# Kernel tuning notes

Measured on AMD Instinct MI355X. Metric: run time of the kernel, lower is better.

## Reference

```python
import jax, jax.numpy as jnp
import numpy as np

B, S, T = 32, 32, 64          # docs, sentences/doc, tokens/sentence
E, HW, HS = 128, 128, 128     # embed, word hidden, sentence hidden
CW, CS = 128, 128             # attention context sizes
V, NC = 50000, 8              # vocab, classes


def setup_inputs() -> dict:
    key = jax.random.key(0)
    ks = iter(jax.random.split(key, 40))
    x = jax.random.randint(next(ks), (B, S, T), 1, V, dtype=jnp.int32)
    wl = jax.random.randint(next(ks), (B, S), 8, T + 1)   # word lengths
    sl = jax.random.randint(next(ks), (B,), 8, S + 1)     # sentence counts
    tmask = jnp.arange(T)[None, None, :] < wl[:, :, None]
    smask = (jnp.arange(S)[None, :] < sl[:, None])[:, :, None]
    x = jnp.where(tmask & smask, x, 0)                     # 0 = pad token

    def u(shape, scale=0.1):
        return jax.random.uniform(next(ks), shape, jnp.float32, -scale, scale)

    d = {"x": x, "emb": u((V, E))}
    # GRU params in torch layout: W_ih [3H,D] (r|z|n), W_hh [3H,H], biases [3H]
    for pre, Din, H in [("wf", E, HW), ("wb", E, HW), ("sf", 2 * HW, HS), ("sb", 2 * HW, HS)]:
        d[pre + "_Wih"] = u((3 * H, Din))
        d[pre + "_Whh"] = u((3 * H, H))
        d[pre + "_bih"] = u((3 * H,))
        d[pre + "_bhh"] = u((3 * H,))
    d["wproj_W"] = u((CW, 2 * HW)); d["wproj_b"] = u((CW,)); d["wctx"] = u((CW,))
    d["sproj_W"] = u((CS, 2 * HS)); d["sproj_b"] = u((CS,)); d["sctx"] = u((CS,))
    d["fc_W"] = u((NC, 2 * HS)); d["fc_b"] = u((NC,))
    return d


def seq_lens_2d(tok):
    # torch get_sequence_lens: T - trailing zeros, 1 if all zero
    nz = tok != 0
    any_nz = jnp.any(nz, axis=1)
    last = tok.shape[1] - jnp.argmax(nz[:, ::-1], axis=1)
    return jnp.where(any_nz, last, 1)


def doc_lens(x):
    # torch get_num_sentences_lens: S - trailing all-zero sentences
    nz = jnp.any(x != 0, axis=2)  # [B,S]
    any_nz = jnp.any(nz, axis=1)
    last = x.shape[1] - jnp.argmax(nz[:, ::-1], axis=1)
    return jnp.where(any_nz, last, 1)


def run_gru(x, lens, Wih, Whh, bih, bhh, reverse):
    # x: [N,Tm,D]; emulates pack_padded: state frozen / output zeroed beyond len
    N, Tm, _ = x.shape
    H = Whh.shape[1]
    xp = jnp.einsum('ntd,gd->ntg', x, Wih) + bih  # [N,Tm,3H]

    def step(h, inp):
        xg, t = inp
        hg = h @ Whh.T + bhh
        xr, xz, xn = jnp.split(xg, 3, axis=-1)
        hr, hz, hn = jnp.split(hg, 3, axis=-1)
        r = jax.nn.sigmoid(xr + hr)
        z = jax.nn.sigmoid(xz + hz)
        n = jnp.tanh(xn + r * hn)
        h_new = (1 - z) * n + z * h
        valid = (t < lens)[:, None]
        h_new = jnp.where(valid, h_new, h)
        return h_new, jnp.where(valid, h_new, 0.0)

    h0 = jnp.zeros((N, H), x.dtype)
    _, ys = jax.lax.scan(step, h0, (jnp.swapaxes(xp, 0, 1), jnp.arange(Tm)), reverse=reverse)
    return jnp.swapaxes(ys, 0, 1)  # [N,Tm,H]


def bigru(x, lens, pf, pb):
    return jnp.concatenate([run_gru(x, lens, *pf, reverse=False),
                            run_gru(x, lens, *pb, reverse=True)], axis=-1)


def attn_pool(out, lens, Wp, bp, ctx):
    # faithful to torch: softmax over padded positions up to max(lens)
    # (pad_packed pads to max length; padded outputs are zero but score=tanh(b)@c)
    Tm = out.shape[1]
    scores = jnp.tanh(out @ Wp.T + bp) @ ctx            # [N,Tm]
    valid = jnp.arange(Tm)[None, :] < jnp.max(lens)
    attn = jax.nn.softmax(jnp.where(valid, scores, -jnp.inf), axis=-1)
    return jnp.einsum('nt,nth->nh', attn, out)


def han_forward(x, emb,
                wf_Wih, wf_Whh, wf_bih, wf_bhh, wb_Wih, wb_Whh, wb_bih, wb_bhh,
                wproj_W, wproj_b, wctx,
                sf_Wih, sf_Whh, sf_bih, sf_bhh, sb_Wih, sb_Whh, sb_bih, sb_bhh,
                sproj_W, sproj_b, sctx, fc_W, fc_b):
    Bx, Sx, Tx = x.shape
    xw = x.reshape(-1, Tx)                      # [B*S, T]
    wlens = seq_lens_2d(xw)
    slens = doc_lens(x)
    we = emb[xw]                                # [B*S, T, E]
    wout = bigru(we, wlens, (wf_Wih, wf_Whh, wf_bih, wf_bhh),
                 (wb_Wih, wb_Whh, wb_bih, wb_bhh))     # [B*S, T, 2HW]
    sent = attn_pool(wout, wlens, wproj_W, wproj_b, wctx)  # [B*S, 2HW]
    sent = sent.reshape(Bx, Sx, -1)
    sout = bigru(sent, slens, (sf_Wih, sf_Whh, sf_bih, sf_bhh),
                 (sb_Wih, sb_Whh, sb_bih, sb_bhh))     # [B, S, 2HS]
    doc = attn_pool(sout, slens, sproj_W, sproj_b, sctx)   # [B, 2HS]
    return doc @ fc_W.T + fc_b                             # [B, NC]


def reference(x, emb,
              wf_Wih, wf_Whh, wf_bih, wf_bhh, wb_Wih, wb_Whh, wb_bih, wb_bhh,
              wproj_W, wproj_b, wctx,
              sf_Wih, sf_Whh, sf_bih, sf_bhh, sb_Wih, sb_Whh, sb_bih, sb_bhh,
              sproj_W, sproj_b, sctx, fc_W, fc_b):
    return han_forward(x, emb,
                       wf_Wih, wf_Whh, wf_bih, wf_bhh, wb_Wih, wb_Whh, wb_bih, wb_bhh,
                       wproj_W, wproj_b, wctx,
                       sf_Wih, sf_Whh, sf_bih, sf_bhh, sb_Wih, sb_Whh, sb_bih, sb_bhh,
                       sproj_W, sproj_b, sctx, fc_W, fc_b)
```

## Files before the change

### kernel.cpp

```cpp
#include <hip/hip_runtime.h>
#include <hip/hip_bf16.h>

typedef unsigned short ushort_t;
typedef __attribute__((ext_vector_type(4))) float floatx4;
typedef __attribute__((ext_vector_type(8))) short short8;

__device__ __forceinline__ float bf2f(ushort_t u) {
    union { unsigned int i; float f; } v; v.i = ((unsigned int)u) << 16; return v.f;
}
__device__ __forceinline__ ushort_t f2bf(float f) {
    union { float f; unsigned int i; } v; v.f = f;
    unsigned int i = v.i;
    i += 0x7fffu + ((i >> 16) & 1u);
    return (ushort_t)(i >> 16);
}
__device__ __forceinline__ float fsig(float x)  { return 1.f / (1.f + __expf(-x)); }
__device__ __forceinline__ float ftanh(float x) { return 1.f - 2.f / (__expf(2.f * x) + 1.f); }

__device__ __forceinline__ floatx4 MFMA16(short8 a, short8 b, floatx4 c) {
    return __builtin_amdgcn_mfma_f32_16x16x32_bf16(a, b, c, 0, 0, 0);
}

__device__ __forceinline__ void bar_lds() {
    asm volatile("s_waitcnt lgkmcnt(0)" ::: "memory");
    __builtin_amdgcn_s_barrier();
}

#define XIDX(c, m) ((((c) * 16) + ((m) ^ ((c) & 15))) * 8)

__global__ __launch_bounds__(64) void lens_kernel(const int* __restrict__ x,
                                                  const unsigned int* __restrict__ raw,
                                                  int* wlens, int* slens, int* dmax,
                                                  int* flag) {
    int b = blockIdx.x, s = threadIdx.x;
    if (b == 32) {
        int c = 0;
        for (int i = 0; i < 16; ++i) {
            unsigned int v = raw[s * 16 + i];
            unsigned int e = (v >> 7) & 0xFFu;
            if (e > 0x7Bu) ++c;
        }
        c += __shfl_xor(c, 1);  c += __shfl_xor(c, 2);  c += __shfl_xor(c, 4);
        c += __shfl_xor(c, 8);  c += __shfl_xor(c, 16); c += __shfl_xor(c, 32);
        if (s == 0) *flag = (c > 64) ? 1 : 0;
        return;
    }
    int last = 0;
    if (s < 32) {
        const int* tok = x + (b * 32 + s) * 64;
        for (int t = 0; t < 64; t += 4) {
            int4 v = *(const int4*)(tok + t);
            if (v.x) last = t + 1;
            if (v.y) last = t + 2;
            if (v.z) last = t + 3;
            if (v.w) last = t + 4;
        }
        wlens[b * 32 + s] = last ? last : 1;
    }
    int len = (s < 32) ? (last ? last : 1) : 0;
    int lm = len;
    for (int off = 32; off; off >>= 1) lm = max(lm, __shfl_xor(lm, off));
    unsigned long long mask = __ballot(s < 32 && last > 0);
    if (s == 0) {
        slens[b] = mask ? (63 - (int)__clzll(mask) + 1) : 1;
        dmax[b] = lm;
    }
}

struct ConvArgs {
    const void* src[25];
    int dstoff[25];
    int count[25];
    int cumblk[26];
};

__global__ __launch_bounds__(256) void convert_kernel(ConvArgs a, ushort_t* __restrict__ dst,
                                                      const int* __restrict__ flag) {
    int b = blockIdx.x;
    int lo = 0, hi = 24;
    while (lo < hi) { int mid = (lo + hi + 1) >> 1; if (a.cumblk[mid] <= b) lo = mid; else hi = mid - 1; }
    int j = lo;
    size_t base = (size_t)(b - a.cumblk[j]) * 2048 + (size_t)threadIdx.x * 8;
    if (base >= (size_t)a.count[j]) return;
    ushort_t* out = dst + a.dstoff[j] + base;
    if (*flag) {
        const float* s = (const float*)a.src[j] + base;
        float4 v0 = *(const float4*)s;
        float4 v1 = *(const float4*)(s + 4);
        union { ushort_t u[8]; uint4 v; } o;
        o.u[0] = f2bf(v0.x); o.u[1] = f2bf(v0.y); o.u[2] = f2bf(v0.z); o.u[3] = f2bf(v0.w);
        o.u[4] = f2bf(v1.x); o.u[5] = f2bf(v1.y); o.u[6] = f2bf(v1.z); o.u[7] = f2bf(v1.w);
        *(uint4*)out = o.v;
    } else {
        *(uint4*)out = *(const uint4*)((const ushort_t*)a.src[j] + base);
    }
}

__global__ __launch_bounds__(512, 2) void word_gru_kernel(
        const int* __restrict__ x, const ushort_t* __restrict__ emb,
        const ushort_t* __restrict__ Wih_f, const ushort_t* __restrict__ Whh_f,
        const ushort_t* __restrict__ bih_f, const ushort_t* __restrict__ bhh_f,
        const ushort_t* __restrict__ Wih_b, const ushort_t* __restrict__ Whh_b,
        const ushort_t* __restrict__ bih_b, const ushort_t* __restrict__ bhh_b,
        const int* __restrict__ lens, ushort_t* __restrict__ out) {
    const int T = 64;
    __shared__ ushort_t h_buf[2][2048];
    __shared__ ushort_t x_buf[2][2048];
    __shared__ float bsum_lds[256];
    __shared__ float bihn_lds[128];
    __shared__ float bhhn_lds[128];
    __shared__ int tok_lds[1024];

    int tid = threadIdx.x;
    int d = blockIdx.y;
    int n0 = blockIdx.x * 16;
    const ushort_t* Wih = d ? Wih_b : Wih_f;
    const ushort_t* Whh = d ? Whh_b : Whh_f;
    const ushort_t* bih = d ? bih_b : bih_f;
    const ushort_t* bhh = d ? bhh_b : bhh_f;
    int lane = tid & 63, wave = tid >> 6;
    int l15 = lane & 15, l4 = (lane >> 4) & 3;
    int jt = wave * 16;
    int j0 = jt + l4 * 4;

    ((int2*)tok_lds)[tid] = ((const int2*)(x + n0 * 64))[tid];
    if (tid < 256) bsum_lds[tid] = bf2f(bih[tid]) + bf2f(bhh[tid]);
    else if (tid < 384) {
        bihn_lds[tid - 256] = bf2f(bih[tid]);
        bhhn_lds[tid - 256] = bf2f(bhh[tid]);
    }
    { uint2 z = {0u, 0u}; *(uint2*)&h_buf[0][tid * 4] = z; }

    short8 wr[4], wz[4], wn[4], ur[4], uz[4], un[4];
    #pragma unroll
    for (int kf = 0; kf < 4; ++kf) {
        int col = kf * 32 + l4 * 8;
        wr[kf] = *(const short8*)(Wih + (size_t)(jt + l15) * 128 + col);
        wz[kf] = *(const short8*)(Wih + (size_t)(128 + jt + l15) * 128 + col);
        wn[kf] = *(const short8*)(Wih + (size_t)(256 + jt + l15) * 128 + col);
        ur[kf] = *(const short8*)(Whh + (size_t)(jt + l15) * 128 + col);
        uz[kf] = *(const short8*)(Whh + (size_t)(128 + jt + l15) * 128 + col);
        un[kf] = *(const short8*)(Whh + (size_t)(256 + jt + l15) * 128 + col);
    }
    __syncthreads();

    floatx4 br  = *(floatx4*)&bsum_lds[j0];
    floatx4 bz  = *(floatx4*)&bsum_lds[128 + j0];
    floatx4 bxn = *(floatx4*)&bihn_lds[j0];
    floatx4 bhn = *(floatx4*)&bhhn_lds[j0];
    int lv = lens[n0 + l15];
    float hreg[4] = {0.f, 0.f, 0.f, 0.f};

    int m_s = tid >> 4, c_s = tid & 15;
    if (tid < 256) {
        int t0 = d ? (T - 1) : 0;
        int tok = tok_lds[m_s * 64 + t0];
        uint4 v = *(const uint4*)(emb + (size_t)tok * 128 + c_s * 8);
        *(uint4*)&x_buf[0][XIDX(c_s, m_s)] = v;
    }
    __syncthreads();

    for (int ti = 0; ti < T; ++ti) {
        int t = d ? (T - 1 - ti) : ti;
        int cur = ti & 1;
        uint4 xnext;
        bool have_next = (ti + 1) < T;
        if (tid < 256 && have_next) {
            int tn = d ? (T - 2 - ti) : (ti + 1);
            xnext = *(const uint4*)(emb + (size_t)tok_lds[m_s * 64 + tn] * 128 + c_s * 8);
        }
        short8 xb[4], hb[4];
        #pragma unroll
        for (int kf = 0; kf < 4; ++kf) {
            xb[kf] = *(const short8*)&x_buf[cur][XIDX(kf * 4 + l4, l15)];
            hb[kf] = *(const short8*)&h_buf[cur][XIDX(kf * 4 + l4, l15)];
        }
        floatx4 arx = br, azx = bz, axn = bxn;
        floatx4 arh = {0.f, 0.f, 0.f, 0.f}, azh = {0.f, 0.f, 0.f, 0.f}, ahn = bhn;
        #pragma unroll
        for (int kf = 0; kf < 4; ++kf) {
            arx = MFMA16(wr[kf], xb[kf], arx);
            azx = MFMA16(wz[kf], xb[kf], azx);
            axn = MFMA16(wn[kf], xb[kf], axn);
        }
        #pragma unroll
        for (int kf = 0; kf < 4; ++kf) {
            arh = MFMA16(ur[kf], hb[kf], arh);
            azh = MFMA16(uz[kf], hb[kf], azh);
            ahn = MFMA16(un[kf], hb[kf], ahn);
        }
        bool valid = t < lv;
        ushort_t hu[4], ou[4];
        #pragma unroll
        for (int i = 0; i < 4; ++i) {
            float r  = fsig(arx[i] + arh[i]);
            float z  = fsig(azx[i] + azh[i]);
            float nn = ftanh(axn[i] + r * ahn[i]);
            float hv = valid ? (nn + z * (hreg[i] - nn)) : hreg[i];
            hreg[i] = hv;
            hu[i] = f2bf(hv);
            ou[i] = valid ? hu[i] : (ushort_t)0;
        }
        ushort4 h4; h4.x = hu[0]; h4.y = hu[1]; h4.z = hu[2]; h4.w = hu[3];
        ushort4 o4; o4.x = ou[0]; o4.y = ou[1]; o4.z = ou[2]; o4.w = ou[3];
        *(ushort4*)&h_buf[cur ^ 1][XIDX(j0 >> 3, l15) + (j0 & 7)] = h4;
        *(ushort4*)(out + ((size_t)(n0 + l15) * T + t) * 256 + d * 128 + j0) = o4;
        if (tid < 256 && have_next)
            *(uint4*)&x_buf[cur ^ 1][XIDX(c_s, m_s)] = xnext;
        bar_lds();
    }
}

__global__ __launch_bounds__(512, 1) void sent_gru_kernel(
        const ushort_t* __restrict__ sent,
        const ushort_t* __restrict__ Wih_f, const ushort_t* __restrict__ Whh_f,
        const ushort_t* __restrict__ bih_f, const ushort_t* __restrict__ bhh_f,
        const ushort_t* __restrict__ Wih_b, const ushort_t* __restrict__ Whh_b,
        const ushort_t* __restrict__ bih_b, const ushort_t* __restrict__ bhh_b,
        const int* __restrict__ lens, ushort_t* __restrict__ out) {
    const int T = 32;
    __shared__ ushort_t h_buf[2][2048];
    __shared__ ushort_t x_buf[2][4096];
    __shared__ float bsum_lds[256];
    __shared__ float bihn_lds[128];
    __shared__ float bhhn_lds[128];

    int tid = threadIdx.x;
    int d = blockIdx.y;
    int n0 = blockIdx.x * 16;
    const ushort_t* Wih = d ? Wih_b : Wih_f;
    const ushort_t* Whh = d ? Whh_b : Whh_f;
    const ushort_t* bih = d ? bih_b : bih_f;
    const ushort_t* bhh = d ? bhh_b : bhh_f;
    int lane = tid & 63, wave = tid >> 6;
    int l15 = lane & 15, l4 = (lane >> 4) & 3;
    int jt = wave * 16;
    int j0 = jt + l4 * 4;

    if (tid < 256) bsum_lds[tid] = bf2f(bih[tid]) + bf2f(bhh[tid]);
    else if (tid < 384) {
        bihn_lds[tid - 256] = bf2f(bih[tid]);
        bhhn_lds[tid - 256] = bf2f(bhh[tid]);
    }
    { uint2 z = {0u, 0u}; *(uint2*)&h_buf[0][tid * 4] = z; }

    short8 wr[8], wz[8], wn[8];
    #pragma unroll
    for (int kf = 0; kf < 8; ++kf) {
        int col = kf * 32 + l4 * 8;
        wr[kf] = *(const short8*)(Wih + (size_t)(jt + l15) * 256 + col);
        wz[kf] = *(const short8*)(Wih + (size_t)(128 + jt + l15) * 256 + col);
        wn[kf] = *(const short8*)(Wih + (size_t)(256 + jt + l15) * 256 + col);
    }
    short8 ur[4], uz[4], un[4];
    #pragma unroll
    for (int kf = 0; kf < 4; ++kf) {
        int col = kf * 32 + l4 * 8;
        ur[kf] = *(const short8*)(Whh + (size_t)(jt + l15) * 128 + col);
        uz[kf] = *(const short8*)(Whh + (size_t)(128 + jt + l15) * 128 + col);
        un[kf] = *(const short8*)(Whh + (size_t)(256 + jt + l15) * 128 + col);
    }
    __syncthreads();

    floatx4 br  = *(floatx4*)&bsum_lds[j0];
    floatx4 bz  = *(floatx4*)&bsum_lds[128 + j0];
    floatx4 bxn = *(floatx4*)&bihn_lds[j0];
    floatx4 bhn = *(floatx4*)&bhhn_lds[j0];
    int lv = lens[n0 + l15];
    float hreg[4] = {0.f, 0.f, 0.f, 0.f};

    int m_x = tid >> 5, c_x = tid & 31;
    {
        int t0 = d ? (T - 1) : 0;
        uint4 v = *(const uint4*)(sent + ((size_t)(n0 + m_x) * T + t0) * 256 + c_x * 8);
        *(uint4*)&x_buf[0][XIDX(c_x, m_x)] = v;
    }
    __syncthreads();

    for (int ti = 0; ti < T; ++ti) {
        int t = d ? (T - 1 - ti) : ti;
        int cur = ti & 1;
        uint4 xnext;
        bool have_next = (ti + 1) < T;
        if (have_next) {
            int tn = d ? (T - 2 - ti) : (ti + 1);
            xnext = *(const uint4*)(sent + ((size_t)(n0 + m_x) * T + tn) * 256 + c_x * 8);
        }
        floatx4 arx = br, azx = bz, axn = bxn;
        floatx4 arh = {0.f, 0.f, 0.f, 0.f}, azh = {0.f, 0.f, 0.f, 0.f}, ahn = bhn;
        #pragma unroll
        for (int kf = 0; kf < 8; ++kf) {
            short8 xb = *(const short8*)&x_buf[cur][XIDX(kf * 4 + l4, l15)];
            arx = MFMA16(wr[kf], xb, arx);
            azx = MFMA16(wz[kf], xb, azx);
            axn = MFMA16(wn[kf], xb, axn);
        }
        #pragma unroll
        for (int kf = 0; kf < 4; ++kf) {
            short8 hb = *(const short8*)&h_buf[cur][XIDX(kf * 4 + l4, l15)];
            arh = MFMA16(ur[kf], hb, arh);
            azh = MFMA16(uz[kf], hb, azh);
            ahn = MFMA16(un[kf], hb, ahn);
        }
        bool valid = t < lv;
        ushort_t hu[4], ou[4];
        #pragma unroll
        for (int i = 0; i < 4; ++i) {
            float r  = fsig(arx[i] + arh[i]);
            float z  = fsig(azx[i] + azh[i]);
            float nn = ftanh(axn[i] + r * ahn[i]);
            float hv = valid ? (nn + z * (hreg[i] - nn)) : hreg[i];
            hreg[i] = hv;
            hu[i] = f2bf(hv);
            ou[i] = valid ? hu[i] : (ushort_t)0;
        }
        ushort4 h4; h4.x = hu[0]; h4.y = hu[1]; h4.z = hu[2]; h4.w = hu[3];
        ushort4 o4; o4.x = ou[0]; o4.y = ou[1]; o4.z = ou[2]; o4.w = ou[3];
        *(ushort4*)&h_buf[cur ^ 1][XIDX(j0 >> 3, l15) + (j0 & 7)] = h4;
        *(ushort4*)(out + ((size_t)(n0 + l15) * T + t) * 256 + d * 128 + j0) = o4;
        if (have_next)
            *(uint4*)&x_buf[cur ^ 1][XIDX(c_x, m_x)] = xnext;
        bar_lds();
    }
}

#define SP 264
__global__ __launch_bounds__(256) void word_attn_kernel(const ushort_t* __restrict__ wout,
                                                        const ushort_t* __restrict__ W,
                                                        const ushort_t* __restrict__ bias,
                                                        const ushort_t* __restrict__ ctx,
                                                        const int* __restrict__ dmax,
                                                        ushort_t* __restrict__ sent) {
    __shared__ ushort_t tile[64 * SP];
    __shared__ float bc[256];
    __shared__ float sc_lds[64];
    __shared__ float p_lds[64];
    int tid = threadIdx.x, g = blockIdx.x;
    for (int idx = tid; idx < 2048; idx += 256) {
        int row = idx >> 5, k0 = (idx & 31) * 8;
        *(uint4*)&tile[row * SP + k0] = *(const uint4*)(wout + ((size_t)g * 64 + row) * 256 + k0);
    }
    if (tid < 128) bc[tid] = bf2f(bias[tid]);
    else bc[tid] = bf2f(ctx[tid - 128]);
    __syncthreads();
    int lane = tid & 63, wave = tid >> 6;
    int l15 = lane & 15, l4 = (lane >> 4) & 3;
    short8 a[8];
    #pragma unroll
    for (int kf = 0; kf < 8; ++kf)
        a[kf] = *(const short8*)&tile[(wave * 16 + l15) * SP + kf * 32 + l4 * 8];
    floatx4 acc[8];
    #pragma unroll
    for (int nt = 0; nt < 8; ++nt) {
        floatx4 c = {0.f, 0.f, 0.f, 0.f};
        #pragma unroll
        for (int kf = 0; kf < 8; ++kf) {
            short8 b = *(const short8*)(W + (size_t)(nt * 16 + l15) * 256 + kf * 32 + l4 * 8);
            c = MFMA16(a[kf], b, c);
        }
        acc[nt] = c;
    }
    float s[4] = {0.f, 0.f, 0.f, 0.f};
    #pragma unroll
    for (int nt = 0; nt < 8; ++nt) {
        float bv = bc[nt * 16 + l15], cv = bc[128 + nt * 16 + l15];
        #pragma unroll
        for (int i = 0; i < 4; ++i)
            s[i] += ftanh(acc[nt][i] + bv) * cv;
    }
    #pragma unroll
    for (int i = 0; i < 4; ++i) {
        s[i] += __shfl_xor(s[i], 1);
        s[i] += __shfl_xor(s[i], 2);
        s[i] += __shfl_xor(s[i], 4);
        s[i] += __shfl_xor(s[i], 8);
    }
    if (l15 == 0) {
        #pragma unroll
        for (int i = 0; i < 4; ++i) sc_lds[wave * 16 + l4 * 4 + i] = s[i];
    }
    __syncthreads();
    if (tid < 64) {
        int ml = dmax[tid & 31];
        for (int off = 32; off; off >>= 1) ml = max(ml, __shfl_xor(ml, off));
        bool v = tid < ml;
        float sc = v ? sc_lds[tid] : -1e30f;
        float mx = sc;
        for (int off = 32; off; off >>= 1) mx = fmaxf(mx, __shfl_xor(mx, off));
        float e = v ? __expf(sc - mx) : 0.f;
        float sum = e;
        for (int off = 32; off; off >>= 1) sum += __shfl_xor(sum, off);
        p_lds[tid] = e / fmaxf(sum, 1e-30f);
    }
    __syncthreads();
    float acc2 = 0.f;
    for (int t = 0; t < 64; ++t) acc2 += p_lds[t] * bf2f(tile[t * SP + tid]);
    sent[(size_t)g * 256 + tid] = f2bf(acc2);
}

__global__ __launch_bounds__(256) void sent_attn_fc_kernel(const ushort_t* __restrict__ sout,
                                                           const ushort_t* __restrict__ W,
                                                           const ushort_t* __restrict__ bias,
                                                           const ushort_t* __restrict__ ctx,
                                                           const ushort_t* __restrict__ fcW,
                                                           const ushort_t* __restrict__ fcb,
                                                           const int* __restrict__ slens,
                                                           const int* __restrict__ flagp,
                                                           void* __restrict__ outp) {
    __shared__ ushort_t tile[32 * SP];
    __shared__ float bc[256];
    __shared__ float sc_lds[32];
    __shared__ float p_lds[32];
    __shared__ float dv[256];
    int tid = threadIdx.x, g = blockIdx.x;
    for (int idx = tid; idx < 1024; idx += 256) {
        int row = idx >> 5, k0 = (idx & 31) * 8;
        *(uint4*)&tile[row * SP + k0] = *(const uint4*)(sout + ((size_t)g * 32 + row) * 256 + k0);
    }
    if (tid < 128) bc[tid] = bf2f(bias[tid]);
    else bc[tid] = bf2f(ctx[tid - 128]);
    __syncthreads();
    int lane = tid & 63, wave = tid >> 6;
    int l15 = lane & 15, l4 = (lane >> 4) & 3;
    if (wave < 2) {
        short8 a[8];
        #pragma unroll
        for (int kf = 0; kf < 8; ++kf)
            a[kf] = *(const short8*)&tile[(wave * 16 + l15) * SP + kf * 32 + l4 * 8];
        floatx4 acc[8];
        #pragma unroll
        for (int nt = 0; nt < 8; ++nt) {
            floatx4 c = {0.f, 0.f, 0.f, 0.f};
            #pragma unroll
            for (int kf = 0; kf < 8; ++kf) {
                short8 b = *(const short8*)(W + (size_t)(nt * 16 + l15) * 256 + kf * 32 + l4 * 8);
                c = MFMA16(a[kf], b, c);
            }
            acc[nt] = c;
        }
        float s[4] = {0.f, 0.f, 0.f, 0.f};
        #pragma unroll
        for (int nt = 0; nt < 8; ++nt) {
            float bv = bc[nt * 16 + l15], cv = bc[128 + nt * 16 + l15];
            #pragma unroll
            for (int i = 0; i < 4; ++i)
                s[i] += ftanh(acc[nt][i] + bv) * cv;
        }
        #pragma unroll
        for (int i = 0; i < 4; ++i) {
            s[i] += __shfl_xor(s[i], 1);
            s[i] += __shfl_xor(s[i], 2);
            s[i] += __shfl_xor(s[i], 4);
            s[i] += __shfl_xor(s[i], 8);
        }
        if (l15 == 0) {
            #pragma unroll
            for (int i = 0; i < 4; ++i) sc_lds[wave * 16 + l4 * 4 + i] = s[i];
        }
    }
    __syncthreads();
    if (tid < 32) {
        int ml = slens[tid];
        for (int off = 16; off; off >>= 1) ml = max(ml, __shfl_xor(ml, off, 32));
        bool v = tid < ml;
        float sc = v ? sc_lds[tid] : -1e30f;
        float mx = sc;
        for (int off = 16; off; off >>= 1) mx = fmaxf(mx, __shfl_xor(mx, off, 32));
        float e = v ? __expf(sc - mx) : 0.f;
        float sum = e;
        for (int off = 16; off; off >>= 1) sum += __shfl_xor(sum, off, 32);
        p_lds[tid] = e / fmaxf(sum, 1e-30f);
    }
    __syncthreads();
    float acc2 = 0.f;
    for (int t = 0; t < 32; ++t) acc2 += p_lds[t] * bf2f(tile[t * SP + tid]);
    dv[tid] = acc2;
    __syncthreads();
    int c = tid >> 5, q0 = (tid & 31) * 8;
    float partial = 0.f;
    #pragma unroll
    for (int q = 0; q < 8; ++q)
        partial += dv[q0 + q] * bf2f(fcW[(size_t)c * 256 + q0 + q]);
    for (int off = 16; off; off >>= 1) partial += __shfl_xor(partial, off, 32);
    if ((tid & 31) == 0) {
        float v = partial + bf2f(fcb[c]);
        if (*flagp) ((float*)outp)[g * 8 + c] = v;
        else        ((ushort_t*)outp)[g * 8 + c] = f2bf(v);
    }
}

extern "C" void kernel_launch(void* const* d_in, const int* in_sizes, int n_in,
                              void* d_out, int out_size, void* d_ws, size_t ws_size,
                              hipStream_t stream) {
    const int* x = (const int*)d_in[0];
    char* ws = (char*)d_ws;

    const size_t O_CONV = 0;
    const size_t O_WOUT = 14680064;
    const size_t O_SENT = 48234496;
    const size_t O_SOUT = 48758784;
    const size_t O_LENS = 49283072;
    const size_t O_SLEN = 49287168;
    const size_t O_DMAX = 49287296;
    const size_t O_FLAG = 49287424;

    ushort_t* conv = (ushort_t*)(ws + O_CONV);
    ushort_t* wout = (ushort_t*)(ws + O_WOUT);
    ushort_t* sent = (ushort_t*)(ws + O_SENT);
    ushort_t* sout = (ushort_t*)(ws + O_SOUT);
    int* wlens = (int*)(ws + O_LENS);
    int* slens = (int*)(ws + O_SLEN);
    int* dmax  = (int*)(ws + O_DMAX);
    int* flag  = (int*)(ws + O_FLAG);

    ConvArgs ca;
    ushort_t* cw[25];
    int off = 0, blk = 0;
    for (int i = 1; i <= 25; ++i) {
        int j = i - 1;
        int cnt = in_sizes[i];
        ca.src[j] = d_in[i];
        ca.dstoff[j] = off;
        ca.count[j] = cnt;
        ca.cumblk[j] = blk;
        cw[j] = conv + off;
        off += cnt;
        blk += (cnt + 2047) / 2048;
    }
    ca.cumblk[25] = blk;

    lens_kernel<<<33, 64, 0, stream>>>(x, (const unsigned int*)d_in[1],
                                       wlens, slens, dmax, flag);
    convert_kernel<<<blk, 256, 0, stream>>>(ca, conv, flag);
    word_gru_kernel<<<dim3(64, 2), 512, 0, stream>>>(
        x, cw[0],
        cw[1], cw[2], cw[3], cw[4],
        cw[5], cw[6], cw[7], cw[8],
        wlens, wout);
    word_attn_kernel<<<1024, 256, 0, stream>>>(wout, cw[17], cw[18], cw[19], dmax, sent);
    sent_gru_kernel<<<dim3(2, 2), 512, 0, stream>>>(
        sent,
        cw[9], cw[10], cw[11], cw[12],
        cw[13], cw[14], cw[15], cw[16],
        slens, sout);
    sent_attn_fc_kernel<<<32, 256, 0, stream>>>(sout, cw[20], cw[21], cw[22],
                                                cw[23], cw[24], slens, flag, d_out);
    (void)n_in; (void)out_size; (void)ws_size;
}
```

Measured before the change: 322.6 us.

## Hoist sentence GRU input projection into parallel GEMM and deepen word-GRU prefetch

```diff
diff --git a/kernel.cpp b/kernel.cpp
--- a/kernel.cpp
+++ b/kernel.cpp
@@ -105,7 +105,7 @@
         const int* __restrict__ lens, ushort_t* __restrict__ out) {
     const int T = 64;
     __shared__ ushort_t h_buf[2][2048];
-    __shared__ ushort_t x_buf[2][2048];
+    __shared__ ushort_t x_buf[3][2048];
     __shared__ float bsum_lds[256];
     __shared__ float bihn_lds[128];
     __shared__ float bhhn_lds[128];
@@ -152,28 +152,31 @@
     float hreg[4] = {0.f, 0.f, 0.f, 0.f};
 
     int m_s = tid >> 4, c_s = tid & 15;
-    if (tid < 256) {
+    bool stg = tid < 256;
+    uint4 pend1, pend2;
+    if (stg) {
         int t0 = d ? (T - 1) : 0;
-        int tok = tok_lds[m_s * 64 + t0];
-        uint4 v = *(const uint4*)(emb + (size_t)tok * 128 + c_s * 8);
+        uint4 v = *(const uint4*)(emb + (size_t)tok_lds[m_s * 64 + t0] * 128 + c_s * 8);
         *(uint4*)&x_buf[0][XIDX(c_s, m_s)] = v;
+    }
+    if (stg && T > 1) {
+        int t1 = d ? (T - 2) : 1;
+        pend1 = *(const uint4*)(emb + (size_t)tok_lds[m_s * 64 + t1] * 128 + c_s * 8);
     }
     __syncthreads();
 
     for (int ti = 0; ti < T; ++ti) {
         int t = d ? (T - 1 - ti) : ti;
-        int cur = ti & 1;
-        uint4 xnext;
-        bool have_next = (ti + 1) < T;
-        if (tid < 256 && have_next) {
-            int tn = d ? (T - 2 - ti) : (ti + 1);
-            xnext = *(const uint4*)(emb + (size_t)tok_lds[m_s * 64 + tn] * 128 + c_s * 8);
+        int cur = ti % 3;
+        if (stg && (ti + 2) < T) {
+            int tn = d ? (T - 3 - ti) : (ti + 2);
+            pend2 = *(const uint4*)(emb + (size_t)tok_lds[m_s * 64 + tn] * 128 + c_s * 8);
         }
         short8 xb[4], hb[4];
         #pragma unroll
         for (int kf = 0; kf < 4; ++kf) {
             xb[kf] = *(const short8*)&x_buf[cur][XIDX(kf * 4 + l4, l15)];
-            hb[kf] = *(const short8*)&h_buf[cur][XIDX(kf * 4 + l4, l15)];
+            hb[kf] = *(const short8*)&h_buf[ti & 1][XIDX(kf * 4 + l4, l15)];
         }
         floatx4 arx = br, azx = bz, axn = bxn;
         floatx4 arh = {0.f, 0.f, 0.f, 0.f}, azh = {0.f, 0.f, 0.f, 0.f}, ahn = bhn;
@@ -203,55 +206,100 @@
         }
         ushort4 h4; h4.x = hu[0]; h4.y = hu[1]; h4.z = hu[2]; h4.w = hu[3];
         ushort4 o4; o4.x = ou[0]; o4.y = ou[1]; o4.z = ou[2]; o4.w = ou[3];
-        *(ushort4*)&h_buf[cur ^ 1][XIDX(j0 >> 3, l15) + (j0 & 7)] = h4;
+        *(ushort4*)&h_buf[(ti & 1) ^ 1][XIDX(j0 >> 3, l15) + (j0 & 7)] = h4;
         *(ushort4*)(out + ((size_t)(n0 + l15) * T + t) * 256 + d * 128 + j0) = o4;
-        if (tid < 256 && have_next)
-            *(uint4*)&x_buf[cur ^ 1][XIDX(c_s, m_s)] = xnext;
+        if (stg && (ti + 1) < T) {
+            *(uint4*)&x_buf[(ti + 1) % 3][XIDX(c_s, m_s)] = pend1;
+            pend1 = pend2;
+        }
         bar_lds();
     }
 }
 
+__global__ __launch_bounds__(256) void spt_gemm_kernel(const ushort_t* __restrict__ A,
+                                                       const ushort_t* __restrict__ Bf_,
+                                                       const ushort_t* __restrict__ biasf,
+                                                       ushort_t* __restrict__ Tf_,
+                                                       const ushort_t* __restrict__ Bb_,
+                                                       const ushort_t* __restrict__ biasb,
+                                                       ushort_t* __restrict__ Tb_) {
+    __shared__ ushort_t As[64 * 256];
+    __shared__ ushort_t Bs[64 * 256];
+    const int K = 256;
+    int tid = threadIdx.x;
+    int by = blockIdx.y;
+    bool sb = by >= 6;
+    int n0 = (sb ? by - 6 : by) * 64;
+    const ushort_t* B = sb ? Bb_ : Bf_;
+    const ushort_t* bias = sb ? biasb : biasf;
+    ushort_t* Tp = sb ? Tb_ : Tf_;
+    int m0 = blockIdx.x * 64;
+    for (int idx = tid; idx < 2048; idx += 256) {
+        int m = idx & 63, c = idx >> 6;
+        *(uint4*)&As[(c * 64 + m) * 8] = *(const uint4*)(A + (size_t)(m0 + m) * K + c * 8);
+    }
+    for (int idx = tid; idx < 2048; idx += 256) {
+        int n = idx & 63, c = idx >> 6;
+        *(uint4*)&Bs[(c * 64 + n) * 8] = *(const uint4*)(B + (size_t)(n0 + n) * K + c * 8);
+    }
+    __syncthreads();
+    int lane = tid & 63, wave = tid >> 6;
+    int wm = (wave & 1) * 32, wn = (wave >> 1) * 32;
+    int l15 = lane & 15, l4 = lane >> 4;
+    floatx4 acc[2][2] = {};
+    for (int kf = 0; kf < 8; ++kf) {
+        int c = kf * 4 + l4;
+        short8 a0 = *(const short8*)&As[(c * 64 + wm + l15) * 8];
+        short8 a1 = *(const short8*)&As[(c * 64 + wm + 16 + l15) * 8];
+        short8 b0 = *(const short8*)&Bs[(c * 64 + wn + l15) * 8];
+        short8 b1 = *(const short8*)&Bs[(c * 64 + wn + 16 + l15) * 8];
+        acc[0][0] = MFMA16(a0, b0, acc[0][0]);
+        acc[0][1] = MFMA16(a0, b1, acc[0][1]);
+        acc[1][0] = MFMA16(a1, b0, acc[1][0]);
+        acc[1][1] = MFMA16(a1, b1, acc[1][1]);
+    }
+    for (int nt = 0; nt < 2; ++nt) {
+        int n = n0 + wn + nt * 16 + l15;
+        float bv = bf2f(bias[n]);
+        int jc = n >> 2, ji = n & 3;
+        for (int mt = 0; mt < 2; ++mt) {
+            int mbase = m0 + wm + mt * 16 + l4 * 4;
+            #pragma unroll
+            for (int i = 0; i < 4; ++i) {
+                int m = mbase + i;
+                int doc = m >> 5, t = m & 31;
+                size_t dst = ((size_t)((doc >> 4) * 32 + t) * 96 + jc) * 64
+                           + (doc & 15) * 4 + ji;
+                Tp[dst] = f2bf(acc[mt][nt][i] + bv);
+            }
+        }
+    }
+}
+
 __global__ __launch_bounds__(512, 1) void sent_gru_kernel(
-        const ushort_t* __restrict__ sent,
-        const ushort_t* __restrict__ Wih_f, const ushort_t* __restrict__ Whh_f,
-        const ushort_t* __restrict__ bih_f, const ushort_t* __restrict__ bhh_f,
-        const ushort_t* __restrict__ Wih_b, const ushort_t* __restrict__ Whh_b,
-        const ushort_t* __restrict__ bih_b, const ushort_t* __restrict__ bhh_b,
+        const ushort_t* __restrict__ spT_f, const ushort_t* __restrict__ spT_b,
+        const ushort_t* __restrict__ Whh_f, const ushort_t* __restrict__ Whh_b,
+        const ushort_t* __restrict__ bhh_f, const ushort_t* __restrict__ bhh_b,
         const int* __restrict__ lens, ushort_t* __restrict__ out) {
     const int T = 32;
     __shared__ ushort_t h_buf[2][2048];
-    __shared__ ushort_t x_buf[2][4096];
-    __shared__ float bsum_lds[256];
-    __shared__ float bihn_lds[128];
-    __shared__ float bhhn_lds[128];
+    __shared__ float bhh_lds[384];
 
     int tid = threadIdx.x;
     int d = blockIdx.y;
     int n0 = blockIdx.x * 16;
-    const ushort_t* Wih = d ? Wih_b : Wih_f;
+    const ushort_t* spT = d ? spT_b : spT_f;
     const ushort_t* Whh = d ? Whh_b : Whh_f;
-    const ushort_t* bih = d ? bih_b : bih_f;
     const ushort_t* bhh = d ? bhh_b : bhh_f;
     int lane = tid & 63, wave = tid >> 6;
     int l15 = lane & 15, l4 = (lane >> 4) & 3;
     int jt = wave * 16;
     int j0 = jt + l4 * 4;
-
-    if (tid < 256) bsum_lds[tid] = bf2f(bih[tid]) + bf2f(bhh[tid]);
-    else if (tid < 384) {
-        bihn_lds[tid - 256] = bf2f(bih[tid]);
-        bhhn_lds[tid - 256] = bf2f(bhh[tid]);
-    }
+    int jc = j0 >> 2;
+
+    if (tid < 384) bhh_lds[tid] = bf2f(bhh[tid]);
     { uint2 z = {0u, 0u}; *(uint2*)&h_buf[0][tid * 4] = z; }
 
-    short8 wr[8], wz[8], wn[8];
-    #pragma unroll
-    for (int kf = 0; kf < 8; ++kf) {
-        int col = kf * 32 + l4 * 8;
-        wr[kf] = *(const short8*)(Wih + (size_t)(jt + l15) * 256 + col);
-        wz[kf] = *(const short8*)(Wih + (size_t)(128 + jt + l15) * 256 + col);
-        wn[kf] = *(const short8*)(Wih + (size_t)(256 + jt + l15) * 256 + col);
-    }
     short8 ur[4], uz[4], un[4];
     #pragma unroll
     for (int kf = 0; kf < 4; ++kf) {
@@ -262,53 +310,51 @@
     }
     __syncthreads();
 
-    floatx4 br  = *(floatx4*)&bsum_lds[j0];
-    floatx4 bz  = *(floatx4*)&bsum_lds[128 + j0];
-    floatx4 bxn = *(floatx4*)&bihn_lds[j0];
-    floatx4 bhn = *(floatx4*)&bhhn_lds[j0];
+    floatx4 br  = *(floatx4*)&bhh_lds[j0];
+    floatx4 bz  = *(floatx4*)&bhh_lds[128 + j0];
+    floatx4 bhn = *(floatx4*)&bhh_lds[256 + j0];
     int lv = lens[n0 + l15];
     float hreg[4] = {0.f, 0.f, 0.f, 0.f};
 
-    int m_x = tid >> 5, c_x = tid & 31;
+    const ushort_t* sp = spT + (size_t)(blockIdx.x * 32) * 96 * 64 + l15 * 4;
+    ushort4 xr_c, xz_c, xn_c, xr_n, xz_n, xn_n;
     {
         int t0 = d ? (T - 1) : 0;
-        uint4 v = *(const uint4*)(sent + ((size_t)(n0 + m_x) * T + t0) * 256 + c_x * 8);
-        *(uint4*)&x_buf[0][XIDX(c_x, m_x)] = v;
-    }
-    __syncthreads();
+        size_t rb = (size_t)t0 * 96 * 64;
+        xr_c = *(const ushort4*)(sp + rb + (size_t)jc * 64);
+        xz_c = *(const ushort4*)(sp + rb + (size_t)(32 + jc) * 64);
+        xn_c = *(const ushort4*)(sp + rb + (size_t)(64 + jc) * 64);
+    }
 
     for (int ti = 0; ti < T; ++ti) {
         int t = d ? (T - 1 - ti) : ti;
         int cur = ti & 1;
-        uint4 xnext;
         bool have_next = (ti + 1) < T;
         if (have_next) {
             int tn = d ? (T - 2 - ti) : (ti + 1);
-            xnext = *(const uint4*)(sent + ((size_t)(n0 + m_x) * T + tn) * 256 + c_x * 8);
-        }
-        floatx4 arx = br, azx = bz, axn = bxn;
-        floatx4 arh = {0.f, 0.f, 0.f, 0.f}, azh = {0.f, 0.f, 0.f, 0.f}, ahn = bhn;
-        #pragma unroll
-        for (int kf = 0; kf < 8; ++kf) {
-            short8 xb = *(const short8*)&x_buf[cur][XIDX(kf * 4 + l4, l15)];
-            arx = MFMA16(wr[kf], xb, arx);
-            azx = MFMA16(wz[kf], xb, azx);
-            axn = MFMA16(wn[kf], xb, axn);
-        }
+            size_t rb = (size_t)tn * 96 * 64;
+            xr_n = *(const ushort4*)(sp + rb + (size_t)jc * 64);
+            xz_n = *(const ushort4*)(sp + rb + (size_t)(32 + jc) * 64);
+            xn_n = *(const ushort4*)(sp + rb + (size_t)(64 + jc) * 64);
+        }
+        floatx4 ar = br, az = bz, ahn = bhn;
         #pragma unroll
         for (int kf = 0; kf < 4; ++kf) {
             short8 hb = *(const short8*)&h_buf[cur][XIDX(kf * 4 + l4, l15)];
-            arh = MFMA16(ur[kf], hb, arh);
-            azh = MFMA16(uz[kf], hb, azh);
+            ar  = MFMA16(ur[kf], hb, ar);
+            az  = MFMA16(uz[kf], hb, az);
             ahn = MFMA16(un[kf], hb, ahn);
         }
+        float xr[4] = {bf2f(xr_c.x), bf2f(xr_c.y), bf2f(xr_c.z), bf2f(xr_c.w)};
+        float xz[4] = {bf2f(xz_c.x), bf2f(xz_c.y), bf2f(xz_c.z), bf2f(xz_c.w)};
+        float xn[4] = {bf2f(xn_c.x), bf2f(xn_c.y), bf2f(xn_c.z), bf2f(xn_c.w)};
         bool valid = t < lv;
         ushort_t hu[4], ou[4];
         #pragma unroll
         for (int i = 0; i < 4; ++i) {
-            float r  = fsig(arx[i] + arh[i]);
-            float z  = fsig(azx[i] + azh[i]);
-            float nn = ftanh(axn[i] + r * ahn[i]);
+            float r  = fsig(xr[i] + ar[i]);
+            float z  = fsig(xz[i] + az[i]);
+            float nn = ftanh(xn[i] + r * ahn[i]);
             float hv = valid ? (nn + z * (hreg[i] - nn)) : hreg[i];
             hreg[i] = hv;
             hu[i] = f2bf(hv);
@@ -318,8 +364,7 @@
         ushort4 o4; o4.x = ou[0]; o4.y = ou[1]; o4.z = ou[2]; o4.w = ou[3];
         *(ushort4*)&h_buf[cur ^ 1][XIDX(j0 >> 3, l15) + (j0 & 7)] = h4;
         *(ushort4*)(out + ((size_t)(n0 + l15) * T + t) * 256 + d * 128 + j0) = o4;
-        if (have_next)
-            *(uint4*)&x_buf[cur ^ 1][XIDX(c_x, m_x)] = xnext;
+        if (have_next) { xr_c = xr_n; xz_c = xz_n; xn_c = xn_n; }
         bar_lds();
     }
 }
@@ -499,15 +544,19 @@
     const size_t O_WOUT = 14680064;
     const size_t O_SENT = 48234496;
     const size_t O_SOUT = 48758784;
-    const size_t O_LENS = 49283072;
-    const size_t O_SLEN = 49287168;
-    const size_t O_DMAX = 49287296;
-    const size_t O_FLAG = 49287424;
+    const size_t O_SPTF = 49283072;
+    const size_t O_SPTB = 50855936;
+    const size_t O_LENS = 52428800;
+    const size_t O_SLEN = 52432896;
+    const size_t O_DMAX = 52433024;
+    const size_t O_FLAG = 52433152;
 
     ushort_t* conv = (ushort_t*)(ws + O_CONV);
     ushort_t* wout = (ushort_t*)(ws + O_WOUT);
     ushort_t* sent = (ushort_t*)(ws + O_SENT);
     ushort_t* sout = (ushort_t*)(ws + O_SOUT);
+    ushort_t* sptf = (ushort_t*)(ws + O_SPTF);
+    ushort_t* sptb = (ushort_t*)(ws + O_SPTB);
     int* wlens = (int*)(ws + O_LENS);
     int* slens = (int*)(ws + O_SLEN);
     int* dmax  = (int*)(ws + O_DMAX);
@@ -538,11 +587,10 @@
         cw[5], cw[6], cw[7], cw[8],
         wlens, wout);
     word_attn_kernel<<<1024, 256, 0, stream>>>(wout, cw[17], cw[18], cw[19], dmax, sent);
+    spt_gemm_kernel<<<dim3(16, 12), 256, 0, stream>>>(sent, cw[9], cw[11], sptf,
+                                                      cw[13], cw[15], sptb);
     sent_gru_kernel<<<dim3(2, 2), 512, 0, stream>>>(
-        sent,
-        cw[9], cw[10], cw[11], cw[12],
-        cw[13], cw[14], cw[15], cw[16],
-        slens, sout);
+        sptf, sptb, cw[10], cw[14], cw[12], cw[16], slens, sout);
     sent_attn_fc_kernel<<<32, 256, 0, stream>>>(sout, cw[20], cw[21], cw[22],
                                                 cw[23], cw[24], slens, flag, d_out);
     (void)n_in; (void)out_size; (void)ws_size;
```

Measured after the change: 317.6 us. Within noise of the previous version (-1.5%).
